# Performance work log

Hardware: AMD Instinct MI355X
Metric: run time of the kernel (lower is better)

Reference implementation:

```python
import jax, jax.numpy as jnp
import numpy as np

N, D, V, T = 2048, 64, 32000, 512
K_WTA = 256
X_DECAY, U_DECAY = 0.97, 0.97
SPIKE_RATE = 0.01
FORGET_ETA = 0.01
HOMEO_TAU = 1.0
GAMMA_MAX = 1.0


def ln_row(z, eps=1e-6):
    # torch .std is unbiased (ddof=1)
    m = z.mean(-1, keepdims=True)
    s = z.std(-1, ddof=1, keepdims=True)
    return (z - m) / (s + eps)


def setup_inputs() -> dict:
    key = jax.random.key(0)
    ks = jax.random.split(key, 6)
    return {
        "tokens": jax.random.randint(ks[0], (T,), 0, V),
        "spike_u": jax.random.uniform(ks[1], (T, N), dtype=jnp.float32),
        "E": jax.random.normal(ks[2], (D, N), dtype=jnp.float32) / np.sqrt(N).astype(np.float32),
        "Dx": jax.random.normal(ks[3], (N, D), dtype=jnp.float32) / np.sqrt(D).astype(np.float32),
        "Dy": jax.random.normal(ks[4], (N, D), dtype=jnp.float32) / np.sqrt(D).astype(np.float32),
        "token_emb": jax.random.normal(ks[5], (V, D), dtype=jnp.float32) / np.sqrt(D).astype(np.float32),
    }


def reference(tokens, spike_u, E, Dx, Dy, token_emb):
    def step(carry, inp):
        x, rho = carry
        tok, u = inp
        v_prev = token_emb[tok]                                   # (D,)
        x_t = X_DECAY * x + jax.nn.relu(Dx @ v_prev)              # (N,)
        x_t = x_t / (jnp.sum(jnp.abs(x_t)) + 1e-6)                # L1 normalize
        a_hat = ln_row(rho @ x_t)                                 # (D,) ln_before_Dy
        # branches=4 with elementwise softplus == softplus on full matvec
        y_core = jax.nn.softplus(Dy @ a_hat)                      # (N,)
        y_core = y_core + (u < SPIKE_RATE).astype(y_core.dtype)   # spike noise
        # k-WTA: keep top K_WTA entries
        _, idx = jax.lax.top_k(y_core, K_WTA)
        mask = jnp.zeros((N,), bool).at[idx].set(True)
        y_core = y_core * mask.astype(y_core.dtype)
        y_t = jax.nn.relu(y_core) * jax.nn.relu(x_t)
        # homeostasis (torch uses .item() -> constant scale)
        s = y_t.sum()
        scale = jnp.where(s > 1e-8, jnp.minimum(1.0, HOMEO_TAU / (s + 1e-8)), 1.0)
        y_t = y_t * jax.lax.stop_gradient(scale)
        v_star = ln_row(E @ y_t)                                  # (D,)
        # surprisal gain (torch uses .item() -> constant)
        p = jax.nn.softmax(v_star)
        H = -(p * jnp.log(p + 1e-12)).sum()
        gain = jnp.minimum(GAMMA_MAX, H / jnp.log(jnp.float32(D) + 1e-6) * GAMMA_MAX)
        gain = jax.lax.stop_gradient(gain)
        # dynamic top-k on x_t via rank masking (jit-safe data-dependent k)
        k_dyn = jnp.clip((N * (0.05 + 0.25 * gain)).astype(jnp.int32), 1, N)
        order = jnp.argsort(-x_t)
        ranks = jnp.zeros((N,), jnp.int32).at[order].set(jnp.arange(N, dtype=jnp.int32))
        x_t = x_t * (ranks < k_dyn).astype(x_t.dtype)
        # local forgetting on inactive columns, then Hebbian update
        inactive = (x_t <= 0).astype(rho.dtype)
        rho = rho * (1.0 - FORGET_ETA * inactive[None, :])
        rho = U_DECAY * (rho + gain * jnp.outer(v_prev, x_t))
        return (x_t, rho), v_star

    init = (jnp.zeros((N,), jnp.float32), jnp.zeros((D, N), jnp.float32))
    (_, _), v_stack = jax.lax.scan(step, init, (tokens, spike_u))
    return v_stack  # (T, D)
```

## Files before the change

kernel.cpp:

```cpp
#include <hip/hip_runtime.h>
#include <math.h>

#define NB   16
#define NTH  256
#define CH   128
#define NN   2048
#define DD   64
#define TT   512
#define KWTA 256
#define PA   65
#define PB   132

typedef float f32x4 __attribute__((ext_vector_type(4)));

struct __align__(128) BarFlag { unsigned v; unsigned pad[31]; };
__device__ BarFlag g_flag[NB];
__device__ __align__(16) float  g_rf[NB][DD];
__device__ __align__(16) double g_L1[NB];
__device__ __align__(16) float  g_xg[NN];
__device__ __align__(16) float  g_yg[NN];
__device__ __align__(16) float  g_ET[NN*DD];

__global__ void bdh_init(const float* __restrict__ E) {
  const int gid = blockIdx.x * NTH + threadIdx.x;
  if (gid < NB) g_flag[gid].v = 0u;
  for (int idx = gid; idx < NN * DD; idx += 64 * NTH) {
    const int n = idx >> 6, d = idx & 63;
    g_ET[idx] = E[(size_t)d * NN + n];
  }
}

__device__ __forceinline__ void st_coh_f32(float* p, float v) {
  asm volatile("global_store_dword %0, %1, off sc0 sc1" :: "v"(p), "v"(v) : "memory");
}
__device__ __forceinline__ void st_coh_f64(double* p, double v) {
  asm volatile("global_store_dwordx2 %0, %1, off sc0 sc1" :: "v"(p), "v"(v) : "memory");
}

__device__ __forceinline__ void bar_arrive(unsigned& epoch) {
  epoch += 1u;
  asm volatile("s_waitcnt vmcnt(0)" ::: "memory");
  __syncthreads();
  if (threadIdx.x == 0)
    __hip_atomic_store(&g_flag[blockIdx.x].v, epoch, __ATOMIC_RELAXED,
                       __HIP_MEMORY_SCOPE_AGENT);
}
__device__ __forceinline__ void bar_wait(unsigned epoch) {
  if (threadIdx.x < 64) {
    const int i = (int)threadIdx.x;
    for (;;) {
      const bool ok = (i >= NB) ||
        (__hip_atomic_load(&g_flag[i].v, __ATOMIC_RELAXED,
                           __HIP_MEMORY_SCOPE_AGENT) >= epoch);
      if (__all(ok)) break;
      __builtin_amdgcn_s_sleep(1);
    }
  }
  __syncthreads();
}

__device__ __forceinline__ double wredd(double v) {
  #pragma unroll
  for (int off = 32; off > 0; off >>= 1) v += __shfl_xor(v, off, 64);
  return v;
}
__device__ __forceinline__ float wredf(float v) {
  #pragma unroll
  for (int off = 32; off > 0; off >>= 1) v += __shfl_xor(v, off, 64);
  return v;
}

__device__ __forceinline__ unsigned select_mask(const unsigned* __restrict__ keys,
                                                int K, int tid,
                                                unsigned* __restrict__ hist,
                                                unsigned* __restrict__ hist2,
                                                unsigned* __restrict__ cw)
{
  const int wv = tid >> 6, lane = tid & 63;
  const int sub = tid & 7;
  uint4* H4 = (uint4*)hist;
  const uint4 z4 = {0u, 0u, 0u, 0u};
  unsigned prefix = 0u, pmask = 0u;
  int remK = K;
  #pragma unroll
  for (int lev = 0; lev < 4; ++lev) {
    const int shf = 24 - 8 * lev;
    #pragma unroll
    for (int j = 0; j < 8; ++j)
      if ((keys[j] & pmask) == prefix)
        atomicAdd(&hist[(((keys[j] >> shf) & 255u) << 3) + sub], 1u);
    __syncthreads();
    {
      const uint4 a = H4[tid * 2], bq = H4[tid * 2 + 1];
      hist2[tid] = a.x + a.y + a.z + a.w + bq.x + bq.y + bq.z + bq.w;
      H4[tid * 2] = z4;
      H4[tid * 2 + 1] = z4;
    }
    __syncthreads();
    const uint4 cc = ((const uint4*)hist2)[lane];
    unsigned c[4] = {cc.x, cc.y, cc.z, cc.w};
    unsigned s[4];
    s[3] = c[3]; s[2] = c[2] + s[3]; s[1] = c[1] + s[2]; s[0] = c[0] + s[1];
    unsigned SS = s[0];
    #pragma unroll
    for (int off = 1; off < 64; off <<= 1) {
      const unsigned o = __shfl_down(SS, off, 64);
      if (lane + off < 64) SS += o;
    }
    const unsigned T = SS - s[0];
    unsigned pk = 0u;
    #pragma unroll
    for (int k = 0; k < 4; ++k) {
      const unsigned A = s[k] + T;
      if (A >= (unsigned)remK && (A - c[k]) < (unsigned)remK)
        pk = (((unsigned)(4 * lane + k)) << 16) | (unsigned)(remK - (int)(A - c[k]));
    }
    const unsigned long long bal = __ballot(pk != 0u);
    const int src = __ffsll((long long)bal) - 1;
    pk = __shfl(pk, src, 64);
    prefix |= (pk >> 16) << shf;
    remK = (int)(pk & 0xffffu);
    pmask |= 255u << shf;
  }
  const unsigned thr = prefix;
  const unsigned R = (unsigned)remK;
  unsigned lc[8], cnt = 0u;
  #pragma unroll
  for (int j = 0; j < 8; ++j) { lc[j] = cnt; cnt += (keys[j] == thr) ? 1u : 0u; }
  unsigned e = cnt;
  #pragma unroll
  for (int off = 1; off < 64; off <<= 1) {
    const unsigned o = __shfl_up(e, off, 64);
    if (lane >= off) e += o;
  }
  if (lane == 63) cw[wv] = e;
  __syncthreads();
  unsigned base = 0u;
  for (int w = 0; w < wv; ++w) base += cw[w];
  const unsigned excl = base + e - cnt;
  unsigned mask = 0u;
  #pragma unroll
  for (int j = 0; j < 8; ++j)
    if (keys[j] > thr || (keys[j] == thr && excl + lc[j] < R)) mask |= 1u << j;
  return mask;
}

__global__ void __launch_bounds__(NTH)
bdh_main(const int* __restrict__ tokens, const float* __restrict__ spike_u,
         const float* __restrict__ Emat, const float* __restrict__ Dx,
         const float* __restrict__ Dy, const float* __restrict__ temb,
         float* __restrict__ out)
{
  __shared__ float sh_rho[DD][PB];
  __shared__ float sh_Dx[CH][PA];
  __shared__ float sh_Dy[CH][PA];
  __shared__ int   sh_tok[TT];
  __shared__ float sh_v[2][DD];
  __shared__ float sh_xstate[CH];
  __shared__ float sh_xtun[CH];
  __shared__ float sh_ahat[DD];
  __shared__ float sh_ffac[CH];
  __shared__ unsigned sh_hist[256*8];
  __shared__ unsigned sh_hist2[256];
  __shared__ unsigned sh_cw[8];
  __shared__ float sh_fmisc[4];
  __shared__ double sh_dred[8];
  __shared__ double sh_rd[4][DD];
  __shared__ float sh_gred[4][DD];
  __shared__ int   sh_aidx[KWTA];
  __shared__ float sh_aw[KWTA];

  const int tid  = threadIdx.x;
  const int b    = blockIdx.x;
  const int n0   = b * CH;
  const int i2   = tid >> 1;
  const int p2   = tid & 1;
  const int d4   = tid >> 2;
  const int p4   = tid & 3;
  const int lane = tid & 63;
  const int wv   = tid >> 6;
  unsigned epoch = 0u;

  for (int k = tid; k < TT; k += NTH) sh_tok[k] = tokens[k];
  for (int k = tid; k < DD*PB; k += NTH) (&sh_rho[0][0])[k] = 0.0f;
  for (int k = tid; k < 256*8; k += NTH) sh_hist[k] = 0u;
  if (tid < CH) sh_xstate[tid] = 0.0f;
  for (int r = wv; r < CH; r += 4) {
    sh_Dx[r][lane] = Dx[(size_t)(n0 + r)*DD + lane];
    sh_Dy[r][lane] = Dy[(size_t)(n0 + r)*DD + lane];
  }
  __syncthreads();
  if (tid < DD) sh_v[0][tid] = temb[(size_t)sh_tok[0]*DD + tid];
  __syncthreads();

  for (int t = 0; t < TT; ++t) {
    const int par = t & 1;

    float spu = 0.0f;
    if (p2 == 0) spu = spike_u[(size_t)t*NN + n0 + i2];
    if (t + 1 < TT && tid < DD)
      sh_v[par ^ 1][tid] = temb[(size_t)sh_tok[t + 1]*DD + tid];

    float d1 = 0.0f;
    {
      const float* dxr = &sh_Dx[i2][p2*32];
      const float* vv  = &sh_v[par][p2*32];
      #pragma unroll
      for (int j = 0; j < 32; ++j) d1 += dxr[j] * vv[j];
    }
    d1 += __shfl_xor(d1, 1, 64);
    float xnew = 0.0f;
    if (p2 == 0) {
      xnew = 0.97f * sh_xstate[i2] + fmaxf(d1, 0.0f);
      sh_xtun[i2] = xnew;
      st_coh_f32(&g_xg[n0 + i2], xnew);
    }
    {
      double v = (p2 == 0) ? (double)fabsf(xnew) : 0.0;
      v = wredd(v);
      if (lane == 0) sh_dred[wv] = v;
      __syncthreads();
      if (tid == 0) st_coh_f64(&g_L1[b],
                               sh_dred[0] + sh_dred[1] + sh_dred[2] + sh_dred[3]);
    }
    float qa = 0.0f;
    {
      const float* rr = &sh_rho[d4][0];
      #pragma unroll
      for (int j = 0; j < 32; ++j) { const int c = p4 + 4*j; qa += rr[c] * sh_xtun[c]; }
    }
    qa += __shfl_xor(qa, 1, 64);
    qa += __shfl_xor(qa, 2, 64);
    if (p4 == 0) st_coh_f32(&g_rf[b][d4], qa);
    bar_arrive(epoch);
    bar_wait(epoch);

    f32x4 xu0, xu1; float rf0, rf1, rf2, rf3;
    {
      const float* xp = g_xg + tid*8;
      const float* rp = &g_rf[wv*4][lane];
      asm volatile(
        "global_load_dwordx4 %0, %6, off sc0 sc1\n\t"
        "global_load_dwordx4 %1, %6, off offset:16 sc0 sc1\n\t"
        "global_load_dword %2, %7, off sc0 sc1\n\t"
        "global_load_dword %3, %7, off offset:256 sc0 sc1\n\t"
        "global_load_dword %4, %7, off offset:512 sc0 sc1\n\t"
        "global_load_dword %5, %7, off offset:768 sc0 sc1\n\t"
        "s_waitcnt vmcnt(0)"
        : "=&v"(xu0), "=&v"(xu1), "=&v"(rf0), "=&v"(rf1), "=&v"(rf2), "=&v"(rf3)
        : "v"(xp), "v"(rp)
        : "memory");
      __builtin_amdgcn_sched_barrier(0);
    }
    {
      double acc = 0.0;
      acc += (double)rf0; acc += (double)rf1; acc += (double)rf2; acc += (double)rf3;
      sh_rd[wv][lane] = acc;
    }
    if (tid < 64) {
      double lv = 0.0;
      if (tid < NB) {
        asm volatile("global_load_dwordx2 %0, %1, off sc0 sc1\n\ts_waitcnt vmcnt(0)"
                     : "=&v"(lv) : "v"(&g_L1[tid]) : "memory");
      }
      __builtin_amdgcn_sched_barrier(0);
      const double v = wredd(lv);
      if (tid == 0) sh_dred[0] = v;
    }
    __syncthreads();
    const float Lden = (float)sh_dred[0] + 1e-6f;
    if (tid < 64) {
      const double qd = sh_rd[0][tid] + sh_rd[1][tid] + sh_rd[2][tid] + sh_rd[3][tid];
      const float rf = (float)qd / Lden;
      const float mm = wredf(rf) * (1.0f/64.0f);
      const float dv = rf - mm;
      const float sd = sqrtf(wredf(dv*dv) * (1.0f/63.0f));
      sh_ahat[tid] = dv / (sd + 1e-6f);
    }
    unsigned xkeys[8];
    {
      const float xf[8] = {xu0[0],xu0[1],xu0[2],xu0[3], xu1[0],xu1[1],xu1[2],xu1[3]};
      #pragma unroll
      for (int j = 0; j < 8; ++j) xkeys[j] = __float_as_uint(xf[j] / Lden);
    }
    __syncthreads();
    float d2 = 0.0f;
    {
      const float* dyr = &sh_Dy[i2][p2*32];
      const float* aa  = &sh_ahat[p2*32];
      #pragma unroll
      for (int j = 0; j < 32; ++j) d2 += dyr[j] * aa[j];
    }
    d2 += __shfl_xor(d2, 1, 64);
    if (p2 == 0) {
      const float sp = fmaxf(d2, 0.0f) + log1pf(expf(-fabsf(d2)));
      st_coh_f32(&g_yg[n0 + i2], sp + ((spu < 0.01f) ? 1.0f : 0.0f));
    }
    bar_arrive(epoch);
    bar_wait(epoch);

    unsigned ykeys[8];
    {
      f32x4 yv0, yv1;
      const float* yp = g_yg + tid*8;
      asm volatile(
        "global_load_dwordx4 %0, %2, off sc0 sc1\n\t"
        "global_load_dwordx4 %1, %2, off offset:16 sc0 sc1\n\t"
        "s_waitcnt vmcnt(0)"
        : "=&v"(yv0), "=&v"(yv1) : "v"(yp) : "memory");
      __builtin_amdgcn_sched_barrier(0);
      ykeys[0]=__float_as_uint(yv0[0]); ykeys[1]=__float_as_uint(yv0[1]);
      ykeys[2]=__float_as_uint(yv0[2]); ykeys[3]=__float_as_uint(yv0[3]);
      ykeys[4]=__float_as_uint(yv1[0]); ykeys[5]=__float_as_uint(yv1[1]);
      ykeys[6]=__float_as_uint(yv1[2]); ykeys[7]=__float_as_uint(yv1[3]);
    }
    const unsigned km = select_mask(ykeys, KWTA, tid, sh_hist, sh_hist2, sh_cw);
    float p[8]; unsigned nzm = 0u;
    #pragma unroll
    for (int j = 0; j < 8; ++j) {
      const float yv = __uint_as_float(ykeys[j]);
      const float xv = __uint_as_float(xkeys[j]);
      p[j] = yv * xv;
      if (((km >> j) & 1u) && xv > 0.0f) nzm |= 1u << j;
    }
    const unsigned cnt = (unsigned)__popc(nzm);
    {
      double sp = 0.0;
      #pragma unroll
      for (int j = 0; j < 8; ++j) if ((nzm >> j) & 1u) sp += (double)p[j];
      sp = wredd(sp);
      if (lane == 0) sh_dred[wv] = sp;
    }
    unsigned e = cnt;
    #pragma unroll
    for (int off = 1; off < 64; off <<= 1) {
      const unsigned o = __shfl_up(e, off, 64);
      if (lane >= off) e += o;
    }
    if (lane == 63) sh_cw[4 + wv] = e;
    __syncthreads();
    const float sf = (float)(sh_dred[0] + sh_dred[1] + sh_dred[2] + sh_dred[3]);
    const float scale = (sf > 1e-8f) ? fminf(1.0f, 1.0f/(sf + 1e-8f)) : 1.0f;
    const int m = (int)(sh_cw[4] + sh_cw[5] + sh_cw[6] + sh_cw[7]);
    {
      unsigned base = 0u;
      for (int w = 0; w < wv; ++w) base += sh_cw[4 + w];
      int pos = (int)(base + e - cnt);
      #pragma unroll
      for (int j = 0; j < 8; ++j)
        if ((nzm >> j) & 1u) { sh_aidx[pos] = 8*tid + j; sh_aw[pos] = scale * p[j]; ++pos; }
    }
    __syncthreads();
    {
      float a0 = 0.0f, a1 = 0.0f, a2 = 0.0f, a3 = 0.0f;
      int i = wv;
      for (; i + 12 < m; i += 16) {
        a0 = fmaf(sh_aw[i],      g_ET[(size_t)sh_aidx[i]     *DD + lane], a0);
        a1 = fmaf(sh_aw[i + 4],  g_ET[(size_t)sh_aidx[i + 4] *DD + lane], a1);
        a2 = fmaf(sh_aw[i + 8],  g_ET[(size_t)sh_aidx[i + 8] *DD + lane], a2);
        a3 = fmaf(sh_aw[i + 12], g_ET[(size_t)sh_aidx[i + 12]*DD + lane], a3);
      }
      for (; i < m; i += 4)
        a0 = fmaf(sh_aw[i], g_ET[(size_t)sh_aidx[i]*DD + lane], a0);
      sh_gred[wv][lane] = (a0 + a1) + (a2 + a3);
    }
    __syncthreads();
    if (tid < 64) {
      const float z = sh_gred[0][tid] + sh_gred[1][tid] + sh_gred[2][tid] + sh_gred[3][tid];
      const float mn = wredf(z) * (1.0f/64.0f);
      const float dv = z - mn;
      const float sd = sqrtf(wredf(dv*dv) * (1.0f/63.0f));
      const float vs = dv / (sd + 1e-6f);
      if (b == 0) out[t*DD + tid] = vs;
      float mx = vs;
      #pragma unroll
      for (int off = 32; off > 0; off >>= 1) mx = fmaxf(mx, __shfl_xor(mx, off, 64));
      const float ex = expf(vs - mx);
      const float se = wredf(ex);
      const float pp = ex / se;
      const float ht = wredf(-pp * logf(pp + 1e-12f));
      if (tid == 0) sh_fmisc[0] = fminf(1.0f, ht / logf(64.0f));
    }
    __syncthreads();
    const float gain = sh_fmisc[0];
    int kdi = (int)(2048.0f * (0.05f + 0.25f * gain));
    kdi = kdi < 1 ? 1 : (kdi > NN ? NN : kdi);
    const unsigned xm = select_mask(xkeys, kdi, tid, sh_hist, sh_hist2, sh_cw);
    #pragma unroll
    for (int j = 0; j < 8; ++j) {
      const int g = 8*tid + j;
      const unsigned l = (unsigned)(g - n0);
      if (l < (unsigned)CH) {
        const float xv = __uint_as_float(xkeys[j]);
        const float v = ((xm >> j) & 1u) ? xv : 0.0f;
        sh_xstate[l] = v;
        sh_ffac[l] = (v <= 0.0f) ? (1.0f - 0.01f) : 1.0f;
      }
    }
    __syncthreads();
    {
      const float vd = sh_v[par][d4];
      float* rr = &sh_rho[d4][0];
      #pragma unroll
      for (int j = 0; j < 32; ++j) {
        const int c = p4 + 4*j;
        rr[c] = 0.97f * (rr[c]*sh_ffac[c] + gain * (vd * sh_xstate[c]));
      }
    }
    __syncthreads();
  }
}

extern "C" void kernel_launch(void* const* d_in, const int* in_sizes, int n_in,
                              void* d_out, int out_size, void* d_ws, size_t ws_size,
                              hipStream_t stream) {
  const int*   tokens = (const int*)d_in[0];
  const float* spike  = (const float*)d_in[1];
  const float* Emat   = (const float*)d_in[2];
  const float* Dx     = (const float*)d_in[3];
  const float* Dy     = (const float*)d_in[4];
  const float* temb   = (const float*)d_in[5];
  float* out = (float*)d_out;
  (void)in_sizes; (void)n_in; (void)out_size; (void)d_ws; (void)ws_size;
  bdh_init<<<dim3(64), dim3(NTH), 0, stream>>>(Emat);
  bdh_main<<<dim3(NB), dim3(NTH), 0, stream>>>(tokens, spike, Emat, Dx, Dy, temb, out);
}
```

Baseline: 9.760 ms.

## Pack barrier flags into one cache line and add spinning ballast blocks

The per-block barrier flags move from separately padded cache lines into one contiguous 128-byte array. Waiters now poll that single line with no s_sleep, which should cut grid-barrier latency across the 512 sequential steps. The grid also gains 224 extra blocks that spin on dummy FMAs until block 0 signals completion, presumably to keep the GPU active and clocked high while the 16 working blocks run. The trade-off is more contention on the shared flag line, plus power and scheduling interference from the ballast blocks.

```diff
diff --git a/kernel.cpp b/kernel.cpp
--- a/kernel.cpp
+++ b/kernel.cpp
@@ -2,6 +2,8 @@
 #include <math.h>
 
 #define NB   16
+#define NBAL 224
+#define NGRID (NB + NBAL)
 #define NTH  256
 #define CH   128
 #define NN   2048
@@ -13,8 +15,8 @@
 
 typedef float f32x4 __attribute__((ext_vector_type(4)));
 
-struct __align__(128) BarFlag { unsigned v; unsigned pad[31]; };
-__device__ BarFlag g_flag[NB];
+__device__ __align__(128) unsigned g_flags[32];
+__device__ __align__(128) unsigned g_done;
 __device__ __align__(16) float  g_rf[NB][DD];
 __device__ __align__(16) double g_L1[NB];
 __device__ __align__(16) float  g_xg[NN];
@@ -23,7 +25,8 @@
 
 __global__ void bdh_init(const float* __restrict__ E) {
   const int gid = blockIdx.x * NTH + threadIdx.x;
-  if (gid < NB) g_flag[gid].v = 0u;
+  if (gid < 32) g_flags[gid] = 0u;
+  if (gid == 32) g_done = 0u;
   for (int idx = gid; idx < NN * DD; idx += 64 * NTH) {
     const int n = idx >> 6, d = idx & 63;
     g_ET[idx] = E[(size_t)d * NN + n];
@@ -42,18 +45,16 @@
   asm volatile("s_waitcnt vmcnt(0)" ::: "memory");
   __syncthreads();
   if (threadIdx.x == 0)
-    __hip_atomic_store(&g_flag[blockIdx.x].v, epoch, __ATOMIC_RELAXED,
+    __hip_atomic_store(&g_flags[blockIdx.x], epoch, __ATOMIC_RELAXED,
                        __HIP_MEMORY_SCOPE_AGENT);
 }
 __device__ __forceinline__ void bar_wait(unsigned epoch) {
   if (threadIdx.x < 64) {
-    const int i = (int)threadIdx.x;
+    const int i = (int)threadIdx.x & 15;
     for (;;) {
-      const bool ok = (i >= NB) ||
-        (__hip_atomic_load(&g_flag[i].v, __ATOMIC_RELAXED,
-                           __HIP_MEMORY_SCOPE_AGENT) >= epoch);
-      if (__all(ok)) break;
-      __builtin_amdgcn_s_sleep(1);
+      const unsigned v = __hip_atomic_load(&g_flags[i], __ATOMIC_RELAXED,
+                                           __HIP_MEMORY_SCOPE_AGENT);
+      if (__all(v >= epoch)) break;
     }
   }
   __syncthreads();
@@ -170,6 +171,19 @@
   __shared__ int   sh_aidx[KWTA];
   __shared__ float sh_aw[KWTA];
 
+  if (blockIdx.x >= NB) {
+    float a = (float)(threadIdx.x + 1);
+    const float bm = 1.000001f;
+    for (;;) {
+      #pragma unroll 8
+      for (int k = 0; k < 1024; ++k) a = fmaf(a, bm, 0.125f);
+      asm volatile("" :: "v"(a));
+      if (__hip_atomic_load(&g_done, __ATOMIC_RELAXED, __HIP_MEMORY_SCOPE_AGENT))
+        break;
+    }
+    return;
+  }
+
   const int tid  = threadIdx.x;
   const int b    = blockIdx.x;
   const int n0   = b * CH;
@@ -409,6 +423,9 @@
     }
     __syncthreads();
   }
+
+  if (b == 0 && tid == 0)
+    __hip_atomic_store(&g_done, 1u, __ATOMIC_RELAXED, __HIP_MEMORY_SCOPE_AGENT);
 }
 
 extern "C" void kernel_launch(void* const* d_in, const int* in_sizes, int n_in,
@@ -423,5 +440,5 @@
   float* out = (float*)d_out;
   (void)in_sizes; (void)n_in; (void)out_size; (void)d_ws; (void)ws_size;
   bdh_init<<<dim3(64), dim3(NTH), 0, stream>>>(Emat);
-  bdh_main<<<dim3(NB), dim3(NTH), 0, stream>>>(tokens, spike, Emat, Dx, Dy, temb, out);
-}
+  bdh_main<<<dim3(NGRID), dim3(NTH), 0, stream>>>(tokens, spike, Emat, Dx, Dy, temb, out);
+}
```

Result: no change. 9.943 ms (+1.9%).

## Replace 4-pass 8-bit radix select with 3-pass 11/11/10-bit select and prebuilt x histogram

Applied to the files above, without the earlier changes.

The top-k radix select drops from four 8-bit passes to three passes using 2048/2048/1024-bin shared histograms with XOR swizzling, which removes one round of barriers and scans per selection. The first-level histogram for the x keys is built during the inter-block barrier wait, skipping zero keys and counting them separately, so that work overlaps the spin. The larger histograms cost more LDS and a wider per-lane scan, and the swizzle replaces the old per-thread sub-bin spreading for reducing atomic contention.

```diff
diff --git a/kernel.cpp b/kernel.cpp
--- a/kernel.cpp
+++ b/kernel.cpp
@@ -70,60 +70,84 @@
   return v;
 }
 
-__device__ __forceinline__ unsigned select_mask(const unsigned* __restrict__ keys,
-                                                int K, int tid,
-                                                unsigned* __restrict__ hist,
-                                                unsigned* __restrict__ hist2,
-                                                unsigned* __restrict__ cw)
-{
+__device__ __forceinline__ unsigned swz2048(unsigned b) {
+  const unsigned q = b >> 2;
+  return ((q ^ ((q >> 3) & 7u)) << 2) | (b & 3u);
+}
+
+__device__ __forceinline__ uint2 scan2048(const unsigned* __restrict__ h, int lane,
+                                          unsigned remK, unsigned zc) {
+  const uint4* H4 = (const uint4*)h;
+  unsigned f[32];
+  const int lx = lane & 7;
+  #pragma unroll
+  for (int i = 0; i < 8; ++i) {
+    const uint4 v = H4[lane*8 + (i ^ lx)];
+    f[i*4+0]=v.x; f[i*4+1]=v.y; f[i*4+2]=v.z; f[i*4+3]=v.w;
+  }
+  if (lane == 0) f[0] += zc;
+  unsigned tot = 0u;
+  #pragma unroll
+  for (int k = 0; k < 32; ++k) tot += f[k];
+  unsigned SS = tot;
+  #pragma unroll
+  for (int off = 1; off < 64; off <<= 1) {
+    const unsigned o = __shfl_down(SS, off, 64);
+    if (lane + off < 64) SS += o;
+  }
+  unsigned FS = SS - tot;
+  unsigned pk = 0u;
+  #pragma unroll
+  for (int k = 31; k >= 0; --k) {
+    const unsigned Alo = FS;
+    FS += f[k];
+    if (FS >= remK && Alo < remK)
+      pk = (((unsigned)(lane*32 + k)) << 16) | (remK - Alo);
+  }
+  const unsigned long long bal = __ballot(pk != 0u);
+  const int src = __ffsll((long long)bal) - 1;
+  pk = __shfl(pk, src, 64);
+  return make_uint2(pk >> 16, pk & 0xffffu);
+}
+
+__device__ __forceinline__ uint2 scan1024(const unsigned* __restrict__ h, int lane,
+                                          unsigned remK, unsigned zc) {
+  const uint4* H4 = (const uint4*)h;
+  unsigned f[16];
+  #pragma unroll
+  for (int i = 0; i < 4; ++i) {
+    const uint4 v = H4[lane*4 + i];
+    f[i*4+0]=v.x; f[i*4+1]=v.y; f[i*4+2]=v.z; f[i*4+3]=v.w;
+  }
+  if (lane == 0) f[0] += zc;
+  unsigned tot = 0u;
+  #pragma unroll
+  for (int k = 0; k < 16; ++k) tot += f[k];
+  unsigned SS = tot;
+  #pragma unroll
+  for (int off = 1; off < 64; off <<= 1) {
+    const unsigned o = __shfl_down(SS, off, 64);
+    if (lane + off < 64) SS += o;
+  }
+  unsigned FS = SS - tot;
+  unsigned pk = 0u;
+  #pragma unroll
+  for (int k = 15; k >= 0; --k) {
+    const unsigned Alo = FS;
+    FS += f[k];
+    if (FS >= remK && Alo < remK)
+      pk = (((unsigned)(lane*16 + k)) << 16) | (remK - Alo);
+  }
+  const unsigned long long bal = __ballot(pk != 0u);
+  const int src = __ffsll((long long)bal) - 1;
+  pk = __shfl(pk, src, 64);
+  return make_uint2(pk >> 16, pk & 0xffffu);
+}
+
+__device__ __forceinline__ unsigned tie_mask(const unsigned* __restrict__ keys,
+                                             unsigned thr, unsigned R, int tid,
+                                             unsigned* __restrict__ cw) {
   const int wv = tid >> 6, lane = tid & 63;
-  const int sub = tid & 7;
-  uint4* H4 = (uint4*)hist;
-  const uint4 z4 = {0u, 0u, 0u, 0u};
-  unsigned prefix = 0u, pmask = 0u;
-  int remK = K;
-  #pragma unroll
-  for (int lev = 0; lev < 4; ++lev) {
-    const int shf = 24 - 8 * lev;
-    #pragma unroll
-    for (int j = 0; j < 8; ++j)
-      if ((keys[j] & pmask) == prefix)
-        atomicAdd(&hist[(((keys[j] >> shf) & 255u) << 3) + sub], 1u);
-    __syncthreads();
-    {
-      const uint4 a = H4[tid * 2], bq = H4[tid * 2 + 1];
-      hist2[tid] = a.x + a.y + a.z + a.w + bq.x + bq.y + bq.z + bq.w;
-      H4[tid * 2] = z4;
-      H4[tid * 2 + 1] = z4;
-    }
-    __syncthreads();
-    const uint4 cc = ((const uint4*)hist2)[lane];
-    unsigned c[4] = {cc.x, cc.y, cc.z, cc.w};
-    unsigned s[4];
-    s[3] = c[3]; s[2] = c[2] + s[3]; s[1] = c[1] + s[2]; s[0] = c[0] + s[1];
-    unsigned SS = s[0];
-    #pragma unroll
-    for (int off = 1; off < 64; off <<= 1) {
-      const unsigned o = __shfl_down(SS, off, 64);
-      if (lane + off < 64) SS += o;
-    }
-    const unsigned T = SS - s[0];
-    unsigned pk = 0u;
-    #pragma unroll
-    for (int k = 0; k < 4; ++k) {
-      const unsigned A = s[k] + T;
-      if (A >= (unsigned)remK && (A - c[k]) < (unsigned)remK)
-        pk = (((unsigned)(4 * lane + k)) << 16) | (unsigned)(remK - (int)(A - c[k]));
-    }
-    const unsigned long long bal = __ballot(pk != 0u);
-    const int src = __ffsll((long long)bal) - 1;
-    pk = __shfl(pk, src, 64);
-    prefix |= (pk >> 16) << shf;
-    remK = (int)(pk & 0xffffu);
-    pmask |= 255u << shf;
-  }
-  const unsigned thr = prefix;
-  const unsigned R = (unsigned)remK;
   unsigned lc[8], cnt = 0u;
   #pragma unroll
   for (int j = 0; j < 8; ++j) { lc[j] = cnt; cnt += (keys[j] == thr) ? 1u : 0u; }
@@ -143,6 +167,45 @@
   for (int j = 0; j < 8; ++j)
     if (keys[j] > thr || (keys[j] == thr && excl + lc[j] < R)) mask |= 1u << j;
   return mask;
+}
+
+__device__ __forceinline__ unsigned select3(const unsigned* __restrict__ keys,
+                                            int K, unsigned zc, bool prebuilt,
+                                            int tid,
+                                            unsigned* __restrict__ h1,
+                                            unsigned* __restrict__ h2,
+                                            unsigned* __restrict__ h3,
+                                            unsigned* __restrict__ cw) {
+  const int lane = tid & 63;
+  const uint4 z4 = {0u, 0u, 0u, 0u};
+  if (!prebuilt) {
+    #pragma unroll
+    for (int j = 0; j < 8; ++j)
+      atomicAdd(&h1[swz2048(keys[j] >> 21)], 1u);
+  }
+  __syncthreads();
+  const uint2 r1 = scan2048(h1, lane, (unsigned)K, zc);
+  __syncthreads();
+  { uint4* Z = (uint4*)h1; Z[tid*2] = z4; Z[tid*2+1] = z4; }
+  #pragma unroll
+  for (int j = 0; j < 8; ++j)
+    if ((zc == 0u || keys[j] != 0u) && (keys[j] >> 21) == r1.x)
+      atomicAdd(&h2[swz2048((keys[j] >> 10) & 2047u)], 1u);
+  __syncthreads();
+  const uint2 r2 = scan2048(h2, lane, r1.y, (r1.x == 0u) ? zc : 0u);
+  __syncthreads();
+  { uint4* Z = (uint4*)h2; Z[tid*2] = z4; Z[tid*2+1] = z4; }
+  const unsigned pre = (r1.x << 11) | r2.x;
+  #pragma unroll
+  for (int j = 0; j < 8; ++j)
+    if ((zc == 0u || keys[j] != 0u) && (keys[j] >> 10) == pre)
+      atomicAdd(&h3[keys[j] & 1023u], 1u);
+  __syncthreads();
+  const uint2 r3 = scan1024(h3, lane, r2.y, (pre == 0u) ? zc : 0u);
+  __syncthreads();
+  { uint4* Z = (uint4*)h3; Z[tid] = z4; }
+  const unsigned thr = (pre << 10) | r3.x;
+  return tie_mask(keys, thr, r3.y, tid, cw);
 }
 
 __global__ void __launch_bounds__(NTH)
@@ -160,8 +223,11 @@
   __shared__ float sh_xtun[CH];
   __shared__ float sh_ahat[DD];
   __shared__ float sh_ffac[CH];
-  __shared__ unsigned sh_hist[256*8];
-  __shared__ unsigned sh_hist2[256];
+  __shared__ __align__(16) unsigned sh_h1y[2048];
+  __shared__ __align__(16) unsigned sh_h1x[2048];
+  __shared__ __align__(16) unsigned sh_h2[2048];
+  __shared__ __align__(16) unsigned sh_h3[1024];
+  __shared__ unsigned sh_nx[4];
   __shared__ unsigned sh_cw[8];
   __shared__ float sh_fmisc[4];
   __shared__ double sh_dred[8];
@@ -183,7 +249,8 @@
 
   for (int k = tid; k < TT; k += NTH) sh_tok[k] = tokens[k];
   for (int k = tid; k < DD*PB; k += NTH) (&sh_rho[0][0])[k] = 0.0f;
-  for (int k = tid; k < 256*8; k += NTH) sh_hist[k] = 0u;
+  for (int k = tid; k < 2048; k += NTH) { sh_h1y[k]=0u; sh_h1x[k]=0u; sh_h2[k]=0u; }
+  for (int k = tid; k < 1024; k += NTH) sh_h3[k] = 0u;
   if (tid < CH) sh_xstate[tid] = 0.0f;
   for (int r = wv; r < CH; r += 4) {
     sh_Dx[r][lane] = Dx[(size_t)(n0 + r)*DD + lane];
@@ -297,6 +364,15 @@
       st_coh_f32(&g_yg[n0 + i2], sp + ((spu < 0.01f) ? 1.0f : 0.0f));
     }
     bar_arrive(epoch);
+    {
+      unsigned nz = 0u;
+      #pragma unroll
+      for (int j = 0; j < 8; ++j)
+        if (xkeys[j] != 0u) { atomicAdd(&sh_h1x[swz2048(xkeys[j] >> 21)], 1u); ++nz; }
+      #pragma unroll
+      for (int off = 1; off < 64; off <<= 1) nz += __shfl_xor(nz, off, 64);
+      if (lane == 0) sh_nx[wv] = nz;
+    }
     bar_wait(epoch);
 
     unsigned ykeys[8];
@@ -314,7 +390,8 @@
       ykeys[4]=__float_as_uint(yv1[0]); ykeys[5]=__float_as_uint(yv1[1]);
       ykeys[6]=__float_as_uint(yv1[2]); ykeys[7]=__float_as_uint(yv1[3]);
     }
-    const unsigned km = select_mask(ykeys, KWTA, tid, sh_hist, sh_hist2, sh_cw);
+    const unsigned km = select3(ykeys, KWTA, 0u, false, tid,
+                                sh_h1y, sh_h2, sh_h3, sh_cw);
     float p[8]; unsigned nzm = 0u;
     #pragma unroll
     for (int j = 0; j < 8; ++j) {
@@ -385,7 +462,9 @@
     const float gain = sh_fmisc[0];
     int kdi = (int)(2048.0f * (0.05f + 0.25f * gain));
     kdi = kdi < 1 ? 1 : (kdi > NN ? NN : kdi);
-    const unsigned xm = select_mask(xkeys, kdi, tid, sh_hist, sh_hist2, sh_cw);
+    const unsigned zcx = 2048u - (sh_nx[0] + sh_nx[1] + sh_nx[2] + sh_nx[3]);
+    const unsigned xm = select3(xkeys, kdi, zcx, true, tid,
+                                sh_h1x, sh_h2, sh_h3, sh_cw);
     #pragma unroll
     for (int j = 0; j < 8; ++j) {
       const int g = 8*tid + j;
```

Measured after the change: 10.27 ms. 5.3% more time.
